# Optimization experiments

Measured on AMD Instinct MI355X. Metric: run time of the kernel, lower is better.

The kernel has to match this reference:

```python
import jax, jax.numpy as jnp
import numpy as np
import math

P = 2
TAU = 1.0
USE_POW = False
ALIGN_W = 1.0
ENTROPY_W = 1.0
EPS = 1e-12


def _pairwise_l2(z):
    # torch.cdist(z, z, p=2): sqrt of squared distances via GEMM decomposition
    sq = jnp.sum(z * z, axis=-1)  # [N]
    d2 = sq[:, None] + sq[None, :] - 2.0 * (z @ z.T)  # [N, N]
    d = jnp.sqrt(jnp.maximum(d2, 0.0))
    return jnp.maximum(d, EPS)  # clamp_min(eps)


def setup_inputs() -> dict:
    key = jax.random.key(0)
    k0, k1 = jax.random.split(key)
    v0 = jax.random.normal(k0, (8192, 256), dtype=jnp.float32)
    v1 = jax.random.normal(k1, (8192, 256), dtype=jnp.float32)
    return {"v0": v0, "v1": v1}


def reference(v0, v1):
    views = [v0, v1]
    n = v0.shape[0]

    # Alignment term: mean Lp distance between matched rows, one pair (0,1)
    diff = v0 - v1
    align = jnp.sqrt(jnp.sum(diff * diff, axis=-1)).mean()  # p=2 norm per row

    # Entropy term: masked logsumexp over within-view pairwise distances
    log_num_neg = math.log(n - 1)
    eye = jnp.eye(n, dtype=bool)
    entropy = jnp.float32(0.0)
    for z in views:
        dist = _pairwise_l2(z)  # [N, N]
        logits = jnp.where(eye, -jnp.inf, -dist / TAU)
        lme = jax.nn.logsumexp(logits, axis=1) - log_num_neg  # [N]
        entropy = entropy + lme.mean()
    entropy = entropy / len(views)

    return ALIGN_W * align + ENTROPY_W * entropy
```

## Files before the change

kernel.cpp:

```cpp
#include <hip/hip_runtime.h>
#include <math.h>


#define D_DIM 256
#define NB 64
#define NSEG 1056
#define S_Q 26.0f
#define LOG2E2 2.0813689810f
#define LP 65

typedef int i32x4 __attribute__((ext_vector_type(4)));
typedef unsigned int u32;
#define AS1 __attribute__((address_space(1)))
#define AS3 __attribute__((address_space(3)))

__device__ inline void load_lds16(const void* g, void* l) {
  __builtin_amdgcn_global_load_lds((const AS1 u32*)g, (AS3 u32*)l, 16, 0, 0);
}

__device__ inline int q8(float x) {
  return __float2int_rn(fminf(fmaxf(x * S_Q, -127.0f), 127.0f));
}
__device__ inline u32 q8x4(const float4 f) {
  return (u32)(q8(f.x) & 255) | ((u32)(q8(f.y) & 255) << 8) |
         ((u32)(q8(f.z) & 255) << 16) | ((u32)(q8(f.w) & 255) << 24);
}

__device__ inline int Gfun(int M) {
  const int m = M >> 1;
  return (M & 1) ? (m + 1) * (m + 1) : m * (m + 1);
}

__global__ __launch_bounds__(256) void prep(
    const float* __restrict__ v0, const float* __restrict__ v1,
    unsigned char* __restrict__ ph0, unsigned char* __restrict__ ph1,
    float* __restrict__ sq0, float* __restrict__ sq1,
    float* __restrict__ S0, float* __restrict__ S1,
    float* __restrict__ align_part,
    double* __restrict__ totals, int* __restrict__ ticket) {
  __shared__ float4 l0[16 * LP], l1[16 * LP];
  __shared__ float red0[4][16], red1[4][16], red2[4][16];
  const int R = blockIdx.x;
  const int t = threadIdx.x;

  if (R == 0 && t == 0) { totals[0] = 0.0; totals[1] = 0.0; ticket[0] = 0; }

  #pragma unroll
  for (int p = 0; p < 4; ++p) {
    const int slot = t + p * 256;
    const int r = slot >> 6, col = slot & 63;
    const size_t g = (size_t)(R * 16 + r) * 64 + col;
    l0[r * LP + col] = ((const float4*)v0)[g];
    l1[r * LP + col] = ((const float4*)v1)[g];
  }
  __syncthreads();

  {
    const int rr = t & 15, c = t >> 4;
    const int s = c >> 2, q = c & 3;
    const int li = rr * LP + c * 4;
    uint4 u0, u1;
    u0.x = q8x4(l0[li + 0]); u0.y = q8x4(l0[li + 1]);
    u0.z = q8x4(l0[li + 2]); u0.w = q8x4(l0[li + 3]);
    u1.x = q8x4(l1[li + 0]); u1.y = q8x4(l1[li + 1]);
    u1.z = q8x4(l1[li + 2]); u1.w = q8x4(l1[li + 3]);
    const size_t dst = (size_t)(R * 4 + s) * 64 + q * 16 + rr;
    ((uint4*)ph0)[dst] = u0;
    ((uint4*)ph1)[dst] = u1;
  }

  {
    const int rr = t & 15;
    const int base = rr * LP + (t >> 4) * 4;
    float s0p = 0.f, s1p = 0.f, s2p = 0.f;
    #pragma unroll
    for (int c = 0; c < 4; ++c) {
      const float4 a = l0[base + c], b = l1[base + c];
      s0p += a.x * a.x + a.y * a.y + a.z * a.z + a.w * a.w;
      s1p += b.x * b.x + b.y * b.y + b.z * b.z + b.w * b.w;
      const float dx = a.x - b.x, dy = a.y - b.y, dz = a.z - b.z, dw = a.w - b.w;
      s2p += dx * dx + dy * dy + dz * dz + dw * dw;
    }
    s0p += __shfl_xor(s0p, 16, 64); s0p += __shfl_xor(s0p, 32, 64);
    s1p += __shfl_xor(s1p, 16, 64); s1p += __shfl_xor(s1p, 32, 64);
    s2p += __shfl_xor(s2p, 16, 64); s2p += __shfl_xor(s2p, 32, 64);
    const int w = t >> 6, lane = t & 63;
    if (lane < 16) { red0[w][lane] = s0p; red1[w][lane] = s1p; red2[w][lane] = s2p; }
  }
  __syncthreads();
  if (t < 16) {
    const int row = R * 16 + t;
    const float a0 = red0[0][t] + red0[1][t] + red0[2][t] + red0[3][t];
    const float a1 = red1[0][t] + red1[1][t] + red1[2][t] + red1[3][t];
    const float a2 = red2[0][t] + red2[1][t] + red2[2][t] + red2[3][t];
    sq0[row] = a0 * LOG2E2;
    sq1[row] = a1 * LOG2E2;
    align_part[row] = sqrtf(a2);
    S0[row] = 0.0f;
    S1[row] = 0.0f;
  }
}

__global__ __launch_bounds__(256) void entropy_tile(
    const unsigned char* __restrict__ ph0, const unsigned char* __restrict__ ph1,
    const float* __restrict__ sq0, const float* __restrict__ sq1,
    float* __restrict__ S0, float* __restrict__ S1) {
  const int bid = blockIdx.x;
  const int oct = bid & 7;
  const int view = (oct >> 2) & 1;
  const int lin = (bid >> 3) * 4 + (oct & 3);

  const unsigned char* __restrict__ ph = view ? ph1 : ph0;
  const float* __restrict__ sq = view ? sq1 : sq0;
  float* __restrict__ S        = view ? S1 : S0;

  int bi = 0;
  while (NSEG - Gfun(64 - (bi + 1)) <= lin) ++bi;
  const int q = lin - (NSEG - Gfun(64 - bi));
  const int bj0 = bi + 2 * q;

  __shared__ __align__(16) char smem[32768];
  float* swp = (float*)smem;

  const int t = threadIdx.x, lane = t & 63, w = t >> 6;
  const int wi = w >> 1, wj = w & 1;
  const int quad = lane >> 4, l15 = lane & 15;
  const int i0 = bi * 128;

  #pragma unroll
  for (int r8 = 0; r8 < 8; ++r8) {
    const int seg = w * 8 + r8;
    const unsigned char* src = ph + (size_t)bi * 32768 + seg * 1024 + lane * 16;
    load_lds16(src, smem + seg * 1024);
  }
  __syncthreads();

  const i32x4* __restrict__ phv = (const i32x4*)ph;
  const i32x4* smemv = (const i32x4*)smem;
  const float K2 = 2.0f * LOG2E2 / (S_Q * S_Q);

  float prow[4][4];
  #pragma unroll
  for (int m = 0; m < 4; ++m)
    #pragma unroll
    for (int r = 0; r < 4; ++r) prow[m][r] = 0.f;

  auto do_tile = [&](const int bj, const bool diag_t) {
    const int j0 = bj * 128;
    const int baseB = ((bj * 8 + wj * 4) * 4) * 64 + lane;

    float sjl[4];
    #pragma unroll
    for (int n = 0; n < 4; ++n) sjl[n] = sq[j0 + wj * 64 + n * 16 + l15];

    float csum[4] = {0.f, 0.f, 0.f, 0.f};

    auto epilogue = [&](const i32x4* acc, const float* si, const int m) {
      #pragma unroll
      for (int r = 0; r < 4; ++r) {
        const int gi = i0 + wi * 64 + m * 16 + quad * 4 + r;
        float p = 0.f;
        #pragma unroll
        for (int n = 0; n < 4; ++n) {
          const float d2 = fmaf(-K2, (float)acc[n][r], si[r] + sjl[n]);
          float e = __builtin_amdgcn_exp2f(-__builtin_amdgcn_sqrtf(d2));
          if (diag_t && gi == j0 + wj * 64 + n * 16 + l15) e = 0.f;
          p += e;
          csum[n] += e;
        }
        prow[m][r] += p;
      }
    };

    #pragma unroll
    for (int p = 0; p < 2; ++p) {
      const int m0 = 2 * p, m1 = m0 + 1;
      float si0[4], si1[4];
      #pragma unroll
      for (int r = 0; r < 4; ++r) {
        si0[r] = sq[i0 + wi * 64 + m0 * 16 + quad * 4 + r];
        si1[r] = sq[i0 + wi * 64 + m1 * 16 + quad * 4 + r];
      }
      i32x4 acc0[4], acc1[4];
      #pragma unroll
      for (int n = 0; n < 4; ++n) {
        acc0[n] = (i32x4){0, 0, 0, 0};
        acc1[n] = (i32x4){0, 0, 0, 0};
      }
      #pragma unroll
      for (int s = 0; s < 4; ++s) {
        i32x4 bf[4];
        #pragma unroll
        for (int n = 0; n < 4; ++n) bf[n] = phv[baseB + (n * 4 + s) * 64];
        const i32x4 ah0 = smemv[(size_t)((wi * 4 + m0) * 4 + s) * 64 + lane];
        const i32x4 ah1 = smemv[(size_t)((wi * 4 + m1) * 4 + s) * 64 + lane];
        #pragma unroll
        for (int n = 0; n < 4; ++n)
          acc0[n] = __builtin_amdgcn_mfma_i32_16x16x64_i8(ah0, bf[n], acc0[n], 0, 0, 0);
        #pragma unroll
        for (int n = 0; n < 4; ++n)
          acc1[n] = __builtin_amdgcn_mfma_i32_16x16x64_i8(ah1, bf[n], acc1[n], 0, 0, 0);
      }
      epilogue(acc0, si0, m0);
      epilogue(acc1, si1, m1);
    }

    if (!diag_t) {
      #pragma unroll
      for (int n = 0; n < 4; ++n) {
        float c2 = csum[n];
        c2 += __shfl_xor(c2, 16, 64);
        c2 += __shfl_xor(c2, 32, 64);
        if (quad == 0) atomicAdd(&S[j0 + wj * 64 + n * 16 + l15], c2);
      }
    }
  };

  if (bj0 == bi) do_tile(bi, true); else do_tile(bj0, false);
  if (bj0 + 1 < NB) do_tile(bj0 + 1, false);

  __syncthreads();

  const int wbase = w * 1088;
  #pragma unroll
  for (int m = 0; m < 4; ++m)
    #pragma unroll
    for (int r = 0; r < 4; ++r)
      swp[wbase + (m * 16 + quad * 4 + r) * 17 + l15] = prow[m][r];
  float rs = 0.f;
  #pragma unroll
  for (int j = 0; j < 16; ++j) rs += swp[wbase + lane * 17 + j];
  atomicAdd(&S[i0 + wi * 64 + lane], rs);
}

__global__ __launch_bounds__(256) void finalize_fused(
    const float* __restrict__ S0, const float* __restrict__ S1,
    const float* __restrict__ align_part,
    double* __restrict__ totals, int* __restrict__ ticket,
    float* __restrict__ out, int n) {
  __shared__ float shl[4], sha[4];
  const int t = threadIdx.x, lane = t & 63, w = t >> 6;
  const int idx = blockIdx.x * 256 + t;
  float lg = __logf(S0[idx]) + __logf(S1[idx]);
  float al = align_part[idx];
  #pragma unroll
  for (int o = 1; o < 64; o <<= 1) {
    lg += __shfl_xor(lg, o, 64);
    al += __shfl_xor(al, o, 64);
  }
  if (lane == 0) { shl[w] = lg; sha[w] = al; }
  __syncthreads();
  if (t == 0) {
    const double pl = (double)(shl[0] + shl[1] + shl[2] + shl[3]);
    const double pa = (double)(sha[0] + sha[1] + sha[2] + sha[3]);
    atomicAdd(&totals[0], pl);
    atomicAdd(&totals[1], pa);
    __threadfence();
    const int old = atomicAdd(ticket, 1);
    if (old == (int)gridDim.x - 1) {
      const double lgt = atomicAdd(&totals[0], 0.0);
      const double alt = atomicAdd(&totals[1], 0.0);
      const double align = alt / (double)n;
      const double entropy = 0.5 * lgt / (double)n - log((double)(n - 1));
      out[0] = (float)(align + entropy);
    }
  }
}

extern "C" void kernel_launch(void* const* d_in, const int* in_sizes, int n_in,
                              void* d_out, int out_size, void* d_ws, size_t ws_size,
                              hipStream_t stream) {
  const float* v0 = (const float*)d_in[0];
  const float* v1 = (const float*)d_in[1];
  float* out = (float*)d_out;
  const int n = in_sizes[0] / D_DIM;

  float* ws         = (float*)d_ws;
  float* sq0        = ws;
  float* sq1        = ws + n;
  float* S0         = ws + 2 * n;
  float* S1         = ws + 3 * n;
  float* align_part = ws + 4 * n;
  double* totals    = (double*)(ws + 5 * n);
  int* ticket       = (int*)(ws + 5 * n + 4);
  unsigned char* ph0 = (unsigned char*)(ws + 5 * n + 64);
  unsigned char* ph1 = ph0 + (size_t)n * D_DIM;

  prep<<<n / 16, 256, 0, stream>>>(v0, v1, ph0, ph1, sq0, sq1, S0, S1,
                                   align_part, totals, ticket);

  entropy_tile<<<2 * NSEG, 256, 0, stream>>>(ph0, ph1, sq0, sq1, S0, S1);

  finalize_fused<<<n / 256, 256, 0, stream>>>(S0, S1, align_part, totals,
                                              ticket, out, n);
}
```

Measured before the change: 111.1 us.

## Split entropy tiles into single-wave 64x64 triangular blocks without LDS

Replaces the 256-thread blocks that each covered a 128-row strip and two 128-column tiles (A staged in LDS) with one 64-thread wavefront per 64x64 upper-triangular tile, reading both A and B operands directly from global memory. The row-sum reduction moves from an LDS transpose to lane shuffles followed by per-row atomics, and the epilogue computes all sqrt values before the exp2 calls. This gives many more small blocks for better load balance and removes LDS traffic and block barriers. The cost is more global/L2 operand reads, less reuse of A, and more atomic operations on S.

```diff
diff --git a/kernel.cpp b/kernel.cpp
--- a/kernel.cpp
+++ b/kernel.cpp
@@ -3,20 +3,14 @@
 
 
 #define D_DIM 256
-#define NB 64
-#define NSEG 1056
+#define NP64 128
+#define NTRI 8256
 #define S_Q 26.0f
 #define LOG2E2 2.0813689810f
 #define LP 65
 
 typedef int i32x4 __attribute__((ext_vector_type(4)));
 typedef unsigned int u32;
-#define AS1 __attribute__((address_space(1)))
-#define AS3 __attribute__((address_space(3)))
-
-__device__ inline void load_lds16(const void* g, void* l) {
-  __builtin_amdgcn_global_load_lds((const AS1 u32*)g, (AS3 u32*)l, 16, 0, 0);
-}
 
 __device__ inline int q8(float x) {
   return __float2int_rn(fminf(fmaxf(x * S_Q, -127.0f), 127.0f));
@@ -24,11 +18,6 @@
 __device__ inline u32 q8x4(const float4 f) {
   return (u32)(q8(f.x) & 255) | ((u32)(q8(f.y) & 255) << 8) |
          ((u32)(q8(f.z) & 255) << 16) | ((u32)(q8(f.w) & 255) << 24);
-}
-
-__device__ inline int Gfun(int M) {
-  const int m = M >> 1;
-  return (M & 1) ? (m + 1) * (m + 1) : m * (m + 1);
 }
 
 __global__ __launch_bounds__(256) void prep(
@@ -101,7 +90,7 @@
   }
 }
 
-__global__ __launch_bounds__(256) void entropy_tile(
+__global__ __launch_bounds__(64) void entropy_tile(
     const unsigned char* __restrict__ ph0, const unsigned char* __restrict__ ph1,
     const float* __restrict__ sq0, const float* __restrict__ sq1,
     float* __restrict__ S0, float* __restrict__ S1) {
@@ -114,57 +103,47 @@
   const float* __restrict__ sq = view ? sq1 : sq0;
   float* __restrict__ S        = view ? S1 : S0;
 
-  int bi = 0;
-  while (NSEG - Gfun(64 - (bi + 1)) <= lin) ++bi;
-  const int q = lin - (NSEG - Gfun(64 - bi));
-  const int bj0 = bi + 2 * q;
-
-  __shared__ __align__(16) char smem[32768];
-  float* swp = (float*)smem;
-
-  const int t = threadIdx.x, lane = t & 63, w = t >> 6;
-  const int wi = w >> 1, wj = w & 1;
+  int i64 = 0;
+  while (128 * (i64 + 1) - ((i64 + 1) * i64) / 2 <= lin) ++i64;
+  const int j64 = i64 + (lin - (128 * i64 - (i64 * (i64 - 1)) / 2));
+  const bool is_diag = (i64 == j64);
+
+  const int lane = threadIdx.x;
   const int quad = lane >> 4, l15 = lane & 15;
-  const int i0 = bi * 128;
-
-  #pragma unroll
-  for (int r8 = 0; r8 < 8; ++r8) {
-    const int seg = w * 8 + r8;
-    const unsigned char* src = ph + (size_t)bi * 32768 + seg * 1024 + lane * 16;
-    load_lds16(src, smem + seg * 1024);
-  }
-  __syncthreads();
+  const int i0 = i64 * 64, j0 = j64 * 64;
 
   const i32x4* __restrict__ phv = (const i32x4*)ph;
-  const i32x4* smemv = (const i32x4*)smem;
+  const int baseA = i64 * 1024 + lane;
+  const int baseB = j64 * 1024 + lane;
   const float K2 = 2.0f * LOG2E2 / (S_Q * S_Q);
 
+  float sjl[4];
+  #pragma unroll
+  for (int n = 0; n < 4; ++n) sjl[n] = sq[j0 + n * 16 + l15];
+
   float prow[4][4];
   #pragma unroll
   for (int m = 0; m < 4; ++m)
     #pragma unroll
     for (int r = 0; r < 4; ++r) prow[m][r] = 0.f;
-
-  auto do_tile = [&](const int bj, const bool diag_t) {
-    const int j0 = bj * 128;
-    const int baseB = ((bj * 8 + wj * 4) * 4) * 64 + lane;
-
-    float sjl[4];
-    #pragma unroll
-    for (int n = 0; n < 4; ++n) sjl[n] = sq[j0 + wj * 64 + n * 16 + l15];
-
-    float csum[4] = {0.f, 0.f, 0.f, 0.f};
-
+  float csum[4] = {0.f, 0.f, 0.f, 0.f};
+
+  auto body = [&](const bool diag_t) {
     auto epilogue = [&](const i32x4* acc, const float* si, const int m) {
       #pragma unroll
       for (int r = 0; r < 4; ++r) {
-        const int gi = i0 + wi * 64 + m * 16 + quad * 4 + r;
-        float p = 0.f;
+        const int gi = i0 + m * 16 + quad * 4 + r;
+        float dneg[4];
         #pragma unroll
         for (int n = 0; n < 4; ++n) {
           const float d2 = fmaf(-K2, (float)acc[n][r], si[r] + sjl[n]);
-          float e = __builtin_amdgcn_exp2f(-__builtin_amdgcn_sqrtf(d2));
-          if (diag_t && gi == j0 + wj * 64 + n * 16 + l15) e = 0.f;
+          dneg[n] = -__builtin_amdgcn_sqrtf(d2);
+        }
+        float p = 0.f;
+        #pragma unroll
+        for (int n = 0; n < 4; ++n) {
+          float e = __builtin_amdgcn_exp2f(dneg[n]);
+          if (diag_t && gi == j0 + n * 16 + l15) e = 0.f;
           p += e;
           csum[n] += e;
         }
@@ -178,8 +157,8 @@
       float si0[4], si1[4];
       #pragma unroll
       for (int r = 0; r < 4; ++r) {
-        si0[r] = sq[i0 + wi * 64 + m0 * 16 + quad * 4 + r];
-        si1[r] = sq[i0 + wi * 64 + m1 * 16 + quad * 4 + r];
+        si0[r] = sq[i0 + m0 * 16 + quad * 4 + r];
+        si1[r] = sq[i0 + m1 * 16 + quad * 4 + r];
       }
       i32x4 acc0[4], acc1[4];
       #pragma unroll
@@ -192,8 +171,8 @@
         i32x4 bf[4];
         #pragma unroll
         for (int n = 0; n < 4; ++n) bf[n] = phv[baseB + (n * 4 + s) * 64];
-        const i32x4 ah0 = smemv[(size_t)((wi * 4 + m0) * 4 + s) * 64 + lane];
-        const i32x4 ah1 = smemv[(size_t)((wi * 4 + m1) * 4 + s) * 64 + lane];
+        const i32x4 ah0 = phv[baseA + (m0 * 4 + s) * 64];
+        const i32x4 ah1 = phv[baseA + (m1 * 4 + s) * 64];
         #pragma unroll
         for (int n = 0; n < 4; ++n)
           acc0[n] = __builtin_amdgcn_mfma_i32_16x16x64_i8(ah0, bf[n], acc0[n], 0, 0, 0);
@@ -204,33 +183,38 @@
       epilogue(acc0, si0, m0);
       epilogue(acc1, si1, m1);
     }
-
-    if (!diag_t) {
-      #pragma unroll
-      for (int n = 0; n < 4; ++n) {
-        float c2 = csum[n];
-        c2 += __shfl_xor(c2, 16, 64);
-        c2 += __shfl_xor(c2, 32, 64);
-        if (quad == 0) atomicAdd(&S[j0 + wj * 64 + n * 16 + l15], c2);
-      }
-    }
   };
 
-  if (bj0 == bi) do_tile(bi, true); else do_tile(bj0, false);
-  if (bj0 + 1 < NB) do_tile(bj0 + 1, false);
-
-  __syncthreads();
-
-  const int wbase = w * 1088;
+  if (is_diag) body(true); else body(false);
+
+  if (!is_diag) {
+    #pragma unroll
+    for (int n = 0; n < 4; ++n) {
+      float c2 = csum[n];
+      c2 += __shfl_xor(c2, 16, 64);
+      c2 += __shfl_xor(c2, 32, 64);
+      if (quad == 0) atomicAdd(&S[j0 + n * 16 + l15], c2);
+    }
+  }
+
   #pragma unroll
   for (int m = 0; m < 4; ++m)
     #pragma unroll
-    for (int r = 0; r < 4; ++r)
-      swp[wbase + (m * 16 + quad * 4 + r) * 17 + l15] = prow[m][r];
-  float rs = 0.f;
-  #pragma unroll
-  for (int j = 0; j < 16; ++j) rs += swp[wbase + lane * 17 + j];
-  atomicAdd(&S[i0 + wi * 64 + lane], rs);
+    for (int r = 0; r < 4; ++r) {
+      float v = prow[m][r];
+      v += __shfl_xor(v, 1, 64);
+      v += __shfl_xor(v, 2, 64);
+      v += __shfl_xor(v, 4, 64);
+      v += __shfl_xor(v, 8, 64);
+      prow[m][r] = v;
+    }
+  if (l15 == 0) {
+    #pragma unroll
+    for (int m = 0; m < 4; ++m)
+      #pragma unroll
+      for (int r = 0; r < 4; ++r)
+        atomicAdd(&S[i0 + m * 16 + quad * 4 + r], prow[m][r]);
+  }
 }
 
 __global__ __launch_bounds__(256) void finalize_fused(
@@ -289,7 +273,7 @@
   prep<<<n / 16, 256, 0, stream>>>(v0, v1, ph0, ph1, sq0, sq1, S0, S1,
                                    align_part, totals, ticket);
 
-  entropy_tile<<<2 * NSEG, 256, 0, stream>>>(ph0, ph1, sq0, sq1, S0, S1);
+  entropy_tile<<<2 * NTRI, 64, 0, stream>>>(ph0, ph1, sq0, sq1, S0, S1);
 
   finalize_fused<<<n / 256, 256, 0, stream>>>(S0, S1, align_part, totals,
                                               ticket, out, n);
```

Measured after the change: 173.5 us. 56.3% more time.
